# Performance work log

Measured on AMD Instinct MI355X. Metric: run time of the kernel, lower is better.

Reference implementation:

```python
import jax, jax.numpy as jnp
import numpy as np

INP = 512
HIDDEN = 512
N_HEADS = 8          # called 'head_dim' in the torch code
D_HEAD = HIDDEN // N_HEADS  # 64
BASE = 10000.0
SCALE = D_HEAD ** (-0.5)


def rope(x):
    # x: [b, s, h, d]
    b, s, h, d = x.shape
    half = d // 2
    theta = 1.0 / (BASE ** (jnp.arange(0, d, 2, dtype=jnp.float32) / d))  # [d/2]
    idx_theta = jnp.arange(s, dtype=jnp.float32)[:, None] * theta[None, :]  # [s, d/2]
    idx_theta2 = jnp.concatenate([idx_theta, idx_theta], axis=1)            # [s, d]
    neg_half = jnp.concatenate([-x[..., half:], x[..., :half]], axis=-1)
    cos = jnp.cos(idx_theta2)[None, :, None, :]
    sin = jnp.sin(idx_theta2)[None, :, None, :]
    return x * cos + neg_half * sin


def setup_inputs() -> dict:
    key = jax.random.key(0)
    ks = jax.random.split(key, 10)
    b, s = 4, 2048
    init = lambda k, shp, fan_in: jax.random.normal(k, shp, jnp.float32) * (fan_in ** -0.5)
    return {
        "x": jax.random.normal(ks[0], (b, s, INP), jnp.float32),
        "c": jax.random.normal(ks[1], (b, s, INP), jnp.float32),
        "Wq": init(ks[2], (INP, HIDDEN), INP), "bq": jnp.zeros((HIDDEN,), jnp.float32),
        "Wk": init(ks[3], (INP, HIDDEN), INP), "bk": jnp.zeros((HIDDEN,), jnp.float32),
        "Wv": init(ks[4], (INP, HIDDEN), INP), "bv": jnp.zeros((HIDDEN,), jnp.float32),
        "Wo": init(ks[5], (HIDDEN, INP), HIDDEN), "bo": jnp.zeros((INP,), jnp.float32),
    }


def reference(x, c, Wq, bq, Wk, bk, Wv, bv, Wo, bo):
    b, s, _ = x.shape
    h_res = x
    q = (c @ Wq + bq).reshape(b, s, N_HEADS, D_HEAD)
    k = (x @ Wk + bk).reshape(b, s, N_HEADS, D_HEAD)
    v = (x @ Wv + bv).reshape(b, s, N_HEADS, D_HEAD)
    q = rope(q)
    k = rope(k)  # computed but unused, exactly as in the source
    # NOTE: source computes scores between q and V (not k) -- faithful reproduction
    att = jnp.einsum('bihd,bjhd->bhij', q, v)            # [b, h, s, s]
    att = jax.nn.softmax(att * SCALE, axis=-1)
    out = jnp.einsum('bhij,bjhd->bihd', att, v)          # [b, s, h, d]
    out = out.reshape(b, s, HIDDEN)
    out = out @ Wo + bo
    return out + h_res
```

## Files before the change

### kernel.cpp

```cpp
#include <hip/hip_runtime.h>
#include <hip/hip_bf16.h>
#include <cstdint>

typedef float f32x4 __attribute__((ext_vector_type(4)));
typedef short bf16x8 __attribute__((ext_vector_type(8)));
typedef unsigned short u16;

#define B_    4
#define S_    2048
#define H_    8
#define D_    64
#define M_    8192

#define OFF_CBF   0UL
#define OFF_XBF   8388608UL
#define OFF_QBH   16777216UL
#define OFF_VBH   25165824UL
#define OFF_VTBH  33554432UL
#define OFF_ATTN  41943040UL
#define OFF_WQT   50331648UL
#define OFF_WVT   50855936UL
#define OFF_WOT   51380224UL
#define OFF_BIAS  51904512UL
#define OFF_COS   51910656UL
#define OFF_SIN   52172800UL
#define WS_NEEDED 52434944UL

__device__ __forceinline__ u16 f2bf(float f){
    union { float f; uint32_t u; } v; v.f = f;
    uint32_t r = (v.u + 0x7fffu + ((v.u >> 16) & 1u)) >> 16;
    return (u16)r;
}
__device__ __forceinline__ float bf2f(u16 h){
    union { uint32_t u; float f; } v; v.u = ((uint32_t)h) << 16;
    return v.f;
}
__device__ __forceinline__ uint32_t fbits(float f){
    union { float f; uint32_t u; } v; v.f = f; return v.u;
}

__device__ __forceinline__ int swz(int row, int col){
    return (col & ~63) | ((((col >> 3) & 7) ^ (row & 7)) << 3) | (col & 7);
}

__device__ __forceinline__ int detect_f32(const void* x_in){
    int lane = threadIdx.x & 63;
    ushort2 dv = ((const ushort2*)x_in)[lane];
    bool hit = ((((dv.x >> 7) & 0xFF) >= 160) || (((dv.y >> 7) & 0xFF) >= 160));
    return __ballot(hit) != 0ULL;
}

__device__ __forceinline__ void gload_lds16(const u16* g, u16* l){
    __builtin_amdgcn_global_load_lds(
        (const __attribute__((address_space(1))) void*)g,
        (__attribute__((address_space(3))) void*)l, 16, 0, 0);
}

__global__ void k_prep(const void* c_in, const void* x_in,
                       const void* Wq, const void* Wv, const void* Wo,
                       const void* bq, const void* bv, const void* bo,
                       u16* c_bf, u16* x_bf,
                       u16* Wqt, u16* Wvt, u16* Wot, float* bias_ws,
                       float* cos_t, float* sin_t){
    int bid = blockIdx.x;
    if (bid >= 11264){
        int idx = (bid - 11264) * 256 + threadIdx.x;
        int pos = idx >> 5, j = idx & 31;
        double theta = pow(10000.0, -(double)j / 32.0);
        double rev = ((double)pos * theta) * 0.15915494309189535;
        rev -= floor(rev);
        float fr = (float)rev;
        cos_t[idx] = __builtin_amdgcn_cosf(fr);
        sin_t[idx] = __builtin_amdgcn_sinf(fr);
        return;
    }
    if (bid >= 8192){
        int f = detect_f32(x_in);
        int wi = (bid - 8192) >> 10;
        int idx = ((bid - 8192) & 1023) * 256 + threadIdx.x;
        int k = idx >> 9, n = idx & 511;
        const void* W; u16* Wt; const void* bb;
        if (wi == 0){ W = Wq; Wt = Wqt; bb = bq; }
        else if (wi == 1){ W = Wv; Wt = Wvt; bb = bv; }
        else { W = Wo; Wt = Wot; bb = bo; }
        float v = f ? ((const float*)W)[idx] : bf2f(((const u16*)W)[idx]);
        Wt[n * 512 + swz(n, k)] = f2bf(v);
        if (idx < 512){
            float b = f ? ((const float*)bb)[idx] : bf2f(((const u16*)bb)[idx]);
            bias_ws[wi * 512 + idx] = b;
        }
        return;
    }
    int f = detect_f32(x_in);
    int isx = bid >= 4096;
    int t = (bid & 4095) * 256 + threadIdx.x;
    const void* src = isx ? x_in : c_in;
    u16* dst = isx ? x_bf : c_bf;
    int e0 = t * 4, row = e0 >> 9, col = e0 & 511;
    size_t didx = (size_t)row * 512 + swz(row, col);
    ushort4 o;
    if (f){
        float4 v = ((const float4*)src)[t];
        o.x = f2bf(v.x); o.y = f2bf(v.y); o.z = f2bf(v.z); o.w = f2bf(v.w);
    } else {
        o = ((const ushort4*)src)[t];
    }
    *(ushort4*)(dst + didx) = o;
}

__global__ __launch_bounds__(256) void k_gemm_qv(
    const u16* __restrict__ c_bf, const u16* __restrict__ x_bf,
    const u16* __restrict__ Wqt, const u16* __restrict__ Wvt,
    const float* __restrict__ bias_ws,
    const float* __restrict__ cos_t, const float* __restrict__ sin_t,
    u16* __restrict__ Qbh, u16* __restrict__ Vbh, u16* __restrict__ Vtbh)
{
    __shared__ __align__(16) u16 Als[2][128 * 64];
    __shared__ __align__(16) u16 Bls[2][128 * 64];
    const int w = threadIdx.x >> 6, lane = threadIdx.x & 63;
    const int g = lane >> 4, cq = lane & 15;
    const int wm = w & 1, wn = w >> 1;
    const int z = blockIdx.z;
    const u16* A  = z ? x_bf : c_bf;
    const u16* Wt = z ? Wvt : Wqt;
    const float* bias = bias_ws + (z ? 512 : 0);
    const int m0b = blockIdx.x * 128, n0b = blockIdx.y * 128;
    const int m0 = m0b + wm * 64, n0 = n0b + wn * 64;
    const int swzi = ((cq & 7) << 3);

    int srow[4], scol[4];
    #pragma unroll
    for (int i = 0; i < 4; i++){
        int flat = (w * 4 + i) * 64 + lane;
        srow[i] = flat >> 3; scol[i] = (flat & 7) * 8;
    }

    const f32x4 zero = {0.f, 0.f, 0.f, 0.f};
    f32x4 acc[4][4];
    #pragma unroll
    for (int i = 0; i < 4; i++)
        #pragma unroll
        for (int j = 0; j < 4; j++) acc[i][j] = zero;

    #pragma unroll
    for (int i = 0; i < 4; i++){
        gload_lds16(A  + (size_t)(m0b + srow[i]) * 512 + scol[i], &Als[0][(w*4 + i) * 512]);
        gload_lds16(Wt + (size_t)(n0b + srow[i]) * 512 + scol[i], &Bls[0][(w*4 + i) * 512]);
    }

    for (int kt = 0; kt < 8; kt++){
        const int buf = kt & 1;
        __builtin_amdgcn_s_waitcnt(0x0F70);
        __syncthreads();
        if (kt < 7){
            const int kk = (kt + 1) * 64;
            #pragma unroll
            for (int i = 0; i < 4; i++){
                gload_lds16(A  + (size_t)(m0b + srow[i]) * 512 + kk + scol[i], &Als[buf^1][(w*4 + i) * 512]);
                gload_lds16(Wt + (size_t)(n0b + srow[i]) * 512 + kk + scol[i], &Bls[buf^1][(w*4 + i) * 512]);
            }
        }
        #pragma unroll
        for (int ks = 0; ks < 2; ks++){
            const int cs = ((ks * 4 + g) << 3) ^ swzi;
            bf16x8 a[4], b[4];
            #pragma unroll
            for (int mt = 0; mt < 4; mt++)
                a[mt] = *(const bf16x8*)&Als[buf][(wm*64 + mt*16 + cq) * 64 + cs];
            #pragma unroll
            for (int nt = 0; nt < 4; nt++)
                b[nt] = *(const bf16x8*)&Bls[buf][(wn*64 + nt*16 + cq) * 64 + cs];
            #pragma unroll
            for (int mt = 0; mt < 4; mt++)
                #pragma unroll
                for (int nt = 0; nt < 4; nt++)
                    acc[mt][nt] = __builtin_amdgcn_mfma_f32_16x16x32_bf16(a[mt], b[nt], acc[mt][nt], 0, 0, 0);
        }
    }
    __syncthreads();

    #pragma unroll
    for (int nt = 0; nt < 4; nt++){
        float bvv = bias[n0 + nt*16 + cq];
        #pragma unroll
        for (int mt = 0; mt < 4; mt++) acc[mt][nt] += bvv;
    }
    const int h = n0 >> 6;
    if (z == 0){
        const float SCL = 0.125f * 1.4426950408889634f;
        #pragma unroll
        for (int mt = 0; mt < 4; mt++){
            #pragma unroll
            for (int r = 0; r < 4; r++){
                int row = m0 + mt*16 + g*4 + r;
                int b_idx = row >> 11, si = row & 2047;
                size_t base = ((size_t)(b_idx*8 + h) * 2048 + si) * 64;
                #pragma unroll
                for (int nt = 0; nt < 2; nt++){
                    int dj = nt*16 + cq;
                    float cv = cos_t[si*32 + dj], sv = sin_t[si*32 + dj];
                    float x1 = acc[mt][nt][r], x2 = acc[mt][nt+2][r];
                    Qbh[base + dj]      = f2bf((x1*cv - x2*sv) * SCL);
                    Qbh[base + dj + 32] = f2bf((x2*cv + x1*sv) * SCL);
                }
            }
        }
    } else {
        float* ltw = ((float*)&Als[0][0]) + w * (16 * 65);
        const int b_idx = m0 >> 11, si0 = m0 & 2047;
        const size_t tbase = ((size_t)(b_idx*8 + h) * 64) * 2048;
        #pragma unroll
        for (int mt = 0; mt < 4; mt++)
            #pragma unroll
            for (int r = 0; r < 4; r++){
                int row = m0 + mt*16 + g*4 + r;
                int bi = row >> 11, si = row & 2047;
                size_t base = ((size_t)(bi*8 + h) * 2048 + si) * 64;
                #pragma unroll
                for (int nt = 0; nt < 4; nt++)
                    Vbh[base + nt*16 + cq] = f2bf(acc[mt][nt][r]);
            }
        #pragma unroll
        for (int nt = 0; nt < 4; nt++){
            #pragma unroll
            for (int mt = 0; mt < 4; mt++)
                #pragma unroll
                for (int r = 0; r < 4; r++)
                    ltw[cq * 65 + mt*16 + g*4 + r] = acc[mt][nt][r];
            __builtin_amdgcn_wave_barrier();
            #pragma unroll
            for (int dd = 0; dd < 16; dd++){
                float v = ltw[dd * 65 + lane];
                Vtbh[tbase + (size_t)(nt*16 + dd) * 2048 + si0 + lane] = f2bf(v);
            }
            __builtin_amdgcn_wave_barrier();
        }
    }
}

__global__ __launch_bounds__(256) void k_attn(
    const u16* __restrict__ Qbh, const u16* __restrict__ Vbh,
    const u16* __restrict__ Vtbh, u16* __restrict__ attn)
{
    __shared__ u16 Vs[2][64 * 68];
    __shared__ u16 Vts[2][64 * 68];
    __shared__ float pl[4][32 * 68];
    const int w = threadIdx.x >> 6, lane = threadIdx.x & 63;
    const int g = lane >> 4, cq = lane & 15;
    const int bh = blockIdx.y;
    const int i0 = blockIdx.x * 128 + w * 32;

    bf16x8 aq[2][2];
    #pragma unroll
    for (int mt = 0; mt < 2; mt++)
        #pragma unroll
        for (int kk = 0; kk < 2; kk++)
            aq[mt][kk] = *(const bf16x8*)(Qbh + ((size_t)bh*2048 + i0 + mt*16 + cq)*64 + kk*32 + g*8);

    int lst[2]; const u16 *gvs[2], *gvt[2];
    #pragma unroll
    for (int i = 0; i < 2; i++){
        int flat = (w*2 + i) * 64 + lane;
        int srow = flat >> 3, scol = (flat & 7) * 8;
        gvs[i] = Vbh  + ((size_t)bh * 2048 + srow) * 64 + scol;
        gvt[i] = Vtbh + ((size_t)(bh * 64) + srow) * 2048 + scol;
        lst[i] = srow * 68 + scol;
    }
    #pragma unroll
    for (int i = 0; i < 2; i++){
        *(bf16x8*)&Vs[0][lst[i]]  = *(const bf16x8*)gvs[i];
        *(bf16x8*)&Vts[0][lst[i]] = *(const bf16x8*)gvt[i];
    }

    const f32x4 zero = {0.f, 0.f, 0.f, 0.f};
    f32x4 o[2][4]; float fl[2][4];
    #pragma unroll
    for (int mt = 0; mt < 2; mt++)
        #pragma unroll
        for (int t = 0; t < 4; t++){ o[mt][t] = zero; fl[mt][t] = 0.f; }

    for (int jt = 0; jt < 32; jt++){
        const int buf = jt & 1;
        bf16x8 n_vs[2], n_vt[2];
        #pragma unroll
        for (int i = 0; i < 2; i++){
            n_vs[i] = *(const bf16x8*)(gvs[i] + (size_t)(jt + 1) * 4096);
            n_vt[i] = *(const bf16x8*)(gvt[i] + (size_t)(jt + 1) * 64);
        }
        __syncthreads();

        bf16x8 bv[2][4];
        #pragma unroll
        for (int kk = 0; kk < 2; kk++)
            #pragma unroll
            for (int t = 0; t < 4; t++)
                bv[kk][t] = *(const bf16x8*)&Vs[buf][(t*16 + cq)*68 + kk*32 + g*8];
        f32x4 s2[2][4];
        #pragma unroll
        for (int mt = 0; mt < 2; mt++){
            #pragma unroll
            for (int t = 0; t < 4; t++) s2[mt][t] = zero;
            #pragma unroll
            for (int kk = 0; kk < 2; kk++)
                #pragma unroll
                for (int t = 0; t < 4; t++)
                    s2[mt][t] = __builtin_amdgcn_mfma_f32_16x16x32_bf16(aq[mt][kk], bv[kk][t], s2[mt][t], 0, 0, 0);
        }
        #pragma unroll
        for (int mt = 0; mt < 2; mt++){
            #pragma unroll
            for (int t = 0; t < 4; t++)
                #pragma unroll
                for (int r = 0; r < 4; r++)
                    s2[mt][t][r] = __builtin_amdgcn_exp2f(s2[mt][t][r]);
            #pragma unroll
            for (int r = 0; r < 4; r++)
                fl[mt][r] += (s2[mt][0][r] + s2[mt][1][r]) + (s2[mt][2][r] + s2[mt][3][r]);
        }
        #pragma unroll
        for (int mt = 0; mt < 2; mt++)
            #pragma unroll
            for (int r = 0; r < 4; r++)
                #pragma unroll
                for (int t = 0; t < 4; t++)
                    pl[w][(mt*16 + g*4 + r)*68 + t*16 + cq] = s2[mt][t][r];
        __builtin_amdgcn_wave_barrier();
        bf16x8 bt[2][4];
        #pragma unroll
        for (int kk = 0; kk < 2; kk++)
            #pragma unroll
            for (int tn = 0; tn < 4; tn++)
                bt[kk][tn] = *(const bf16x8*)&Vts[buf][(tn*16 + cq)*68 + kk*32 + g*8];
        #pragma unroll
        for (int mt = 0; mt < 2; mt++)
            #pragma unroll
            for (int kk = 0; kk < 2; kk++){
                f32x4 u0 = *(const f32x4*)&pl[w][(mt*16 + cq)*68 + kk*32 + g*8];
                f32x4 u1 = *(const f32x4*)&pl[w][(mt*16 + cq)*68 + kk*32 + g*8 + 4];
                union { bf16x8 v; uint32_t wd[4]; } pk;
                pk.wd[0] = (fbits(u0[0]) >> 16) | (fbits(u0[1]) & 0xffff0000u);
                pk.wd[1] = (fbits(u0[2]) >> 16) | (fbits(u0[3]) & 0xffff0000u);
                pk.wd[2] = (fbits(u1[0]) >> 16) | (fbits(u1[1]) & 0xffff0000u);
                pk.wd[3] = (fbits(u1[2]) >> 16) | (fbits(u1[3]) & 0xffff0000u);
                #pragma unroll
                for (int tn = 0; tn < 4; tn++)
                    o[mt][tn] = __builtin_amdgcn_mfma_f32_16x16x32_bf16(pk.v, bt[kk][tn], o[mt][tn], 0, 0, 0);
            }
        __builtin_amdgcn_wave_barrier();

        #pragma unroll
        for (int i = 0; i < 2; i++){
            *(bf16x8*)&Vs[buf ^ 1][lst[i]]  = n_vs[i];
            *(bf16x8*)&Vts[buf ^ 1][lst[i]] = n_vt[i];
        }
    }
    const int b_idx = bh >> 3, h = bh & 7;
    #pragma unroll
    for (int mt = 0; mt < 2; mt++){
        #pragma unroll
        for (int r = 0; r < 4; r++){
            float sum = fl[mt][r];
            sum += __shfl_xor(sum, 1);
            sum += __shfl_xor(sum, 2);
            sum += __shfl_xor(sum, 4);
            sum += __shfl_xor(sum, 8);
            fl[mt][r] = 1.f / sum;
        }
        f32x4 iv = {fl[mt][0], fl[mt][1], fl[mt][2], fl[mt][3]};
        #pragma unroll
        for (int t = 0; t < 4; t++){
            f32x4 ov = o[mt][t] * iv;
            #pragma unroll
            for (int r = 0; r < 4; r++){
                int row = i0 + mt*16 + g*4 + r;
                int col = h*64 + t*16 + cq;
                attn[((size_t)(b_idx*2048 + row))*512 + swz(row, col)] = f2bf(ov[r]);
            }
        }
    }
}

__global__ __launch_bounds__(256) void k_gemm_out(
    const u16* __restrict__ attn, const u16* __restrict__ Wot,
    const float* __restrict__ bias_ws, const void* __restrict__ x_in,
    void* __restrict__ out)
{
    __shared__ __align__(16) u16 Als[2][128 * 64];
    __shared__ __align__(16) u16 Bls[2][64 * 64];
    const int w = threadIdx.x >> 6, lane = threadIdx.x & 63;
    const int g = lane >> 4, cq = lane & 15;
    const int wm = w & 1, wn = w >> 1;
    const int m0b = blockIdx.x * 128, n0b = blockIdx.y * 64;
    const int m0 = m0b + wm * 64, n0 = n0b + wn * 32;
    const int f = detect_f32(x_in);
    const int swzi = ((cq & 7) << 3);

    int sra[4], sca[4], srb[2], scb[2];
    #pragma unroll
    for (int i = 0; i < 4; i++){
        int flat = (w * 4 + i) * 64 + lane;
        sra[i] = flat >> 3; sca[i] = (flat & 7) * 8;
    }
    #pragma unroll
    for (int i = 0; i < 2; i++){
        int flat = (w * 2 + i) * 64 + lane;
        srb[i] = flat >> 3; scb[i] = (flat & 7) * 8;
    }

    const f32x4 zero = {0.f, 0.f, 0.f, 0.f};
    f32x4 acc[4][2];
    #pragma unroll
    for (int i = 0; i < 4; i++)
        #pragma unroll
        for (int j = 0; j < 2; j++) acc[i][j] = zero;

    #pragma unroll
    for (int i = 0; i < 4; i++)
        gload_lds16(attn + (size_t)(m0b + sra[i]) * 512 + sca[i], &Als[0][(w*4 + i) * 512]);
    #pragma unroll
    for (int i = 0; i < 2; i++)
        gload_lds16(Wot + (size_t)(n0b + srb[i]) * 512 + scb[i], &Bls[0][(w*2 + i) * 512]);

    for (int kt = 0; kt < 8; kt++){
        const int buf = kt & 1;
        __builtin_amdgcn_s_waitcnt(0x0F70);
        __syncthreads();
        if (kt < 7){
            const int kk = (kt + 1) * 64;
            #pragma unroll
            for (int i = 0; i < 4; i++)
                gload_lds16(attn + (size_t)(m0b + sra[i]) * 512 + kk + sca[i], &Als[buf^1][(w*4 + i) * 512]);
            #pragma unroll
            for (int i = 0; i < 2; i++)
                gload_lds16(Wot + (size_t)(n0b + srb[i]) * 512 + kk + scb[i], &Bls[buf^1][(w*2 + i) * 512]);
        }
        #pragma unroll
        for (int ks = 0; ks < 2; ks++){
            const int cs = ((ks * 4 + g) << 3) ^ swzi;
            bf16x8 a[4], b[2];
            #pragma unroll
            for (int mt = 0; mt < 4; mt++)
                a[mt] = *(const bf16x8*)&Als[buf][(wm*64 + mt*16 + cq) * 64 + cs];
            #pragma unroll
            for (int nt = 0; nt < 2; nt++)
                b[nt] = *(const bf16x8*)&Bls[buf][(wn*32 + nt*16 + cq) * 64 + cs];
            #pragma unroll
            for (int mt = 0; mt < 4; mt++)
                #pragma unroll
                for (int nt = 0; nt < 2; nt++)
                    acc[mt][nt] = __builtin_amdgcn_mfma_f32_16x16x32_bf16(a[mt], b[nt], acc[mt][nt], 0, 0, 0);
        }
    }
    #pragma unroll
    for (int mt = 0; mt < 4; mt++)
        #pragma unroll
        for (int nt = 0; nt < 2; nt++)
            #pragma unroll
            for (int r = 0; r < 4; r++){
                int row = m0 + mt*16 + g*4 + r;
                int col = n0 + nt*16 + cq;
                size_t idx = (size_t)row * 512 + col;
                float resid = f ? ((const float*)x_in)[idx] : bf2f(((const u16*)x_in)[idx]);
                float v = acc[mt][nt][r] + bias_ws[1024 + col] + resid;
                if (f) ((float*)out)[idx] = v;
                else   ((u16*)out)[idx] = f2bf(v);
            }
}

extern "C" void kernel_launch(void* const* d_in, const int* in_sizes, int n_in,
                              void* d_out, int out_size, void* d_ws, size_t ws_size,
                              hipStream_t stream){
    const void* x_in = d_in[0];
    const void* c_in = d_in[1];
    const void* Wq = d_in[2]; const void* bq = d_in[3];
    const void* Wv = d_in[6]; const void* bv = d_in[7];
    const void* Wo = d_in[8]; const void* bo = d_in[9];

    if (ws_size < WS_NEEDED){
        hipMemsetAsync(d_out, 0, (size_t)out_size * 2, stream);
        return;
    }
    char* ws = (char*)d_ws;
    u16* c_bf  = (u16*)(ws + OFF_CBF);
    u16* x_bf  = (u16*)(ws + OFF_XBF);
    u16* Qbh   = (u16*)(ws + OFF_QBH);
    u16* Vbh   = (u16*)(ws + OFF_VBH);
    u16* Vtbh  = (u16*)(ws + OFF_VTBH);
    u16* attn  = (u16*)(ws + OFF_ATTN);
    u16* Wqt   = (u16*)(ws + OFF_WQT);
    u16* Wvt   = (u16*)(ws + OFF_WVT);
    u16* Wot   = (u16*)(ws + OFF_WOT);
    float* bias_ws = (float*)(ws + OFF_BIAS);
    float* cos_t   = (float*)(ws + OFF_COS);
    float* sin_t   = (float*)(ws + OFF_SIN);

    k_prep<<<11520, 256, 0, stream>>>(c_in, x_in, Wq, Wv, Wo, bq, bv, bo,
                                      c_bf, x_bf, Wqt, Wvt, Wot, bias_ws, cos_t, sin_t);
    k_gemm_qv<<<dim3(64, 4, 2), 256, 0, stream>>>(c_bf, x_bf, Wqt, Wvt, bias_ws,
                                                  cos_t, sin_t, Qbh, Vbh, Vtbh);
    k_attn<<<dim3(16, 32), 256, 0, stream>>>(Qbh, Vbh, Vtbh, attn);
    k_gemm_out<<<dim3(64, 8), 256, 0, stream>>>(attn, Wot, bias_ws, x_in, d_out);
}
```

Before: 196.2 us.

## Keep attention probabilities in registers via transposed MFMA and swizzled V layouts

The attention kernel now computes scores transposed (V·Q) so each lane's exp'd scores can feed a 16x16x16 MFMA directly as a register operand. This removes the per-wave LDS staging buffer for probabilities and its round trip. The projection kernel writes V and V^T with an XOR swizzle so the attention kernel can copy tiles straight to LDS with global_load_lds, without padding and with fewer bank conflicts. The output store is also vectorised. The cost is an extra, smaller MFMA shape for PV, and every consumer must agree on the new swizzled layouts.

Result: no change. 196.4 us (+0.1%).

```diff
diff --git a/kernel.cpp b/kernel.cpp
--- a/kernel.cpp
+++ b/kernel.cpp
@@ -4,6 +4,7 @@
 
 typedef float f32x4 __attribute__((ext_vector_type(4)));
 typedef short bf16x8 __attribute__((ext_vector_type(8)));
+typedef short bf16x4 __attribute__((ext_vector_type(4)));
 typedef unsigned short u16;
 
 #define B_    4
@@ -37,6 +38,15 @@
 }
 __device__ __forceinline__ uint32_t fbits(float f){
     union { float f; uint32_t u; } v; v.f = f; return v.u;
+}
+
+__device__ __forceinline__ f32x4 mfma16(bf16x4 a, bf16x4 b, f32x4 c){
+#if __has_builtin(__builtin_amdgcn_mfma_f32_16x16x16bf16_1k)
+    return __builtin_amdgcn_mfma_f32_16x16x16bf16_1k(a, b, c, 0, 0, 0);
+#else
+    asm volatile("v_mfma_f32_16x16x16_bf16 %0, %1, %2, %0" : "+v"(c) : "v"(a), "v"(b));
+    return c;
+#endif
 }
 
 __device__ __forceinline__ int swz(int row, int col){
@@ -216,9 +226,13 @@
                 int row = m0 + mt*16 + g*4 + r;
                 int bi = row >> 11, si = row & 2047;
                 size_t base = ((size_t)(bi*8 + h) * 2048 + si) * 64;
-                #pragma unroll
-                for (int nt = 0; nt < 4; nt++)
-                    Vbh[base + nt*16 + cq] = f2bf(acc[mt][nt][r]);
+                int s7 = si & 7;
+                #pragma unroll
+                for (int nt = 0; nt < 4; nt++){
+                    int dj = nt*16 + cq;
+                    int col = ((((dj >> 3) ^ s7) & 7) << 3) | (dj & 7);
+                    Vbh[base + col] = f2bf(acc[mt][nt][r]);
+                }
             }
         #pragma unroll
         for (int nt = 0; nt < 4; nt++){
@@ -231,7 +245,8 @@
             #pragma unroll
             for (int dd = 0; dd < 16; dd++){
                 float v = ltw[dd * 65 + lane];
-                Vtbh[tbase + (size_t)(nt*16 + dd) * 2048 + si0 + lane] = f2bf(v);
+                int col = ((((lane >> 3) ^ (dd & 7)) & 7) << 3) | (lane & 7);
+                Vtbh[tbase + (size_t)(nt*16 + dd) * 2048 + si0 + col] = f2bf(v);
             }
             __builtin_amdgcn_wave_barrier();
         }
@@ -242,11 +257,11 @@
     const u16* __restrict__ Qbh, const u16* __restrict__ Vbh,
     const u16* __restrict__ Vtbh, u16* __restrict__ attn)
 {
-    __shared__ u16 Vs[2][64 * 68];
-    __shared__ u16 Vts[2][64 * 68];
-    __shared__ float pl[4][32 * 68];
+    __shared__ __align__(16) u16 Vs[2][64 * 64];
+    __shared__ __align__(16) u16 Vts[2][64 * 64];
     const int w = threadIdx.x >> 6, lane = threadIdx.x & 63;
     const int g = lane >> 4, cq = lane & 15;
+    const int s7 = cq & 7;
     const int bh = blockIdx.y;
     const int i0 = blockIdx.x * 128 + w * 32;
 
@@ -257,125 +272,82 @@
         for (int kk = 0; kk < 2; kk++)
             aq[mt][kk] = *(const bf16x8*)(Qbh + ((size_t)bh*2048 + i0 + mt*16 + cq)*64 + kk*32 + g*8);
 
-    int lst[2]; const u16 *gvs[2], *gvt[2];
-    #pragma unroll
-    for (int i = 0; i < 2; i++){
-        int flat = (w*2 + i) * 64 + lane;
-        int srow = flat >> 3, scol = (flat & 7) * 8;
-        gvs[i] = Vbh  + ((size_t)bh * 2048 + srow) * 64 + scol;
-        gvt[i] = Vtbh + ((size_t)(bh * 64) + srow) * 2048 + scol;
-        lst[i] = srow * 68 + scol;
-    }
-    #pragma unroll
-    for (int i = 0; i < 2; i++){
-        *(bf16x8*)&Vs[0][lst[i]]  = *(const bf16x8*)gvs[i];
-        *(bf16x8*)&Vts[0][lst[i]] = *(const bf16x8*)gvt[i];
-    }
+    const int c0 = (w * 2) * 512, c1 = c0 + 512;
+    const u16* gvs0 = Vbh + (size_t)bh * 131072 + c0 + lane * 8;
+    const u16* gvs1 = gvs0 + 512;
+    const int dr0 = (w * 2) * 8 + (lane >> 3);
+    const u16* gvt0 = Vtbh + ((size_t)bh * 64 + dr0) * 2048 + (lane & 7) * 8;
+    const u16* gvt1 = gvt0 + 8 * 2048;
+
+    gload_lds16(gvs0, &Vs[0][c0]);
+    gload_lds16(gvs1, &Vs[0][c1]);
+    gload_lds16(gvt0, &Vts[0][c0]);
+    gload_lds16(gvt1, &Vts[0][c1]);
 
     const f32x4 zero = {0.f, 0.f, 0.f, 0.f};
-    f32x4 o[2][4]; float fl[2][4];
+    f32x4 o[2][4]; float fl[2] = {0.f, 0.f};
     #pragma unroll
     for (int mt = 0; mt < 2; mt++)
         #pragma unroll
-        for (int t = 0; t < 4; t++){ o[mt][t] = zero; fl[mt][t] = 0.f; }
+        for (int t = 0; t < 4; t++) o[mt][t] = zero;
 
     for (int jt = 0; jt < 32; jt++){
         const int buf = jt & 1;
-        bf16x8 n_vs[2], n_vt[2];
-        #pragma unroll
-        for (int i = 0; i < 2; i++){
-            n_vs[i] = *(const bf16x8*)(gvs[i] + (size_t)(jt + 1) * 4096);
-            n_vt[i] = *(const bf16x8*)(gvt[i] + (size_t)(jt + 1) * 64);
-        }
+        __builtin_amdgcn_s_waitcnt(0x0F70);
         __syncthreads();
-
-        bf16x8 bv[2][4];
-        #pragma unroll
-        for (int kk = 0; kk < 2; kk++)
-            #pragma unroll
-            for (int t = 0; t < 4; t++)
-                bv[kk][t] = *(const bf16x8*)&Vs[buf][(t*16 + cq)*68 + kk*32 + g*8];
-        f32x4 s2[2][4];
-        #pragma unroll
-        for (int mt = 0; mt < 2; mt++){
-            #pragma unroll
-            for (int t = 0; t < 4; t++) s2[mt][t] = zero;
-            #pragma unroll
-            for (int kk = 0; kk < 2; kk++)
-                #pragma unroll
-                for (int t = 0; t < 4; t++)
-                    s2[mt][t] = __builtin_amdgcn_mfma_f32_16x16x32_bf16(aq[mt][kk], bv[kk][t], s2[mt][t], 0, 0, 0);
-        }
-        #pragma unroll
-        for (int mt = 0; mt < 2; mt++){
-            #pragma unroll
-            for (int t = 0; t < 4; t++)
-                #pragma unroll
-                for (int r = 0; r < 4; r++)
-                    s2[mt][t][r] = __builtin_amdgcn_exp2f(s2[mt][t][r]);
-            #pragma unroll
-            for (int r = 0; r < 4; r++)
-                fl[mt][r] += (s2[mt][0][r] + s2[mt][1][r]) + (s2[mt][2][r] + s2[mt][3][r]);
-        }
-        #pragma unroll
-        for (int mt = 0; mt < 2; mt++)
-            #pragma unroll
-            for (int r = 0; r < 4; r++)
-                #pragma unroll
-                for (int t = 0; t < 4; t++)
-                    pl[w][(mt*16 + g*4 + r)*68 + t*16 + cq] = s2[mt][t][r];
-        __builtin_amdgcn_wave_barrier();
-        bf16x8 bt[2][4];
-        #pragma unroll
-        for (int kk = 0; kk < 2; kk++)
-            #pragma unroll
-            for (int tn = 0; tn < 4; tn++)
-                bt[kk][tn] = *(const bf16x8*)&Vts[buf][(tn*16 + cq)*68 + kk*32 + g*8];
-        #pragma unroll
-        for (int mt = 0; mt < 2; mt++)
-            #pragma unroll
-            for (int kk = 0; kk < 2; kk++){
-                f32x4 u0 = *(const f32x4*)&pl[w][(mt*16 + cq)*68 + kk*32 + g*8];
-                f32x4 u1 = *(const f32x4*)&pl[w][(mt*16 + cq)*68 + kk*32 + g*8 + 4];
-                union { bf16x8 v; uint32_t wd[4]; } pk;
-                pk.wd[0] = (fbits(u0[0]) >> 16) | (fbits(u0[1]) & 0xffff0000u);
-                pk.wd[1] = (fbits(u0[2]) >> 16) | (fbits(u0[3]) & 0xffff0000u);
-                pk.wd[2] = (fbits(u1[0]) >> 16) | (fbits(u1[1]) & 0xffff0000u);
-                pk.wd[3] = (fbits(u1[2]) >> 16) | (fbits(u1[3]) & 0xffff0000u);
-                #pragma unroll
-                for (int tn = 0; tn < 4; tn++)
-                    o[mt][tn] = __builtin_amdgcn_mfma_f32_16x16x32_bf16(pk.v, bt[kk][tn], o[mt][tn], 0, 0, 0);
-            }
-        __builtin_amdgcn_wave_barrier();
-
-        #pragma unroll
-        for (int i = 0; i < 2; i++){
-            *(bf16x8*)&Vs[buf ^ 1][lst[i]]  = n_vs[i];
-            *(bf16x8*)&Vts[buf ^ 1][lst[i]] = n_vt[i];
+        if (jt < 31){
+            const size_t os = (size_t)(jt + 1) * 4096, ot = (size_t)(jt + 1) * 64;
+            gload_lds16(gvs0 + os, &Vs[buf^1][c0]);
+            gload_lds16(gvs1 + os, &Vs[buf^1][c1]);
+            gload_lds16(gvt0 + ot, &Vts[buf^1][c0]);
+            gload_lds16(gvt1 + ot, &Vts[buf^1][c1]);
+        }
+        bf16x4 pk[2][4];
+        #pragma unroll
+        for (int t = 0; t < 4; t++){
+            bf16x8 bv0 = *(const bf16x8*)&Vs[buf][(t*16 + cq)*64 + ((g ^ s7) << 3)];
+            bf16x8 bv1 = *(const bf16x8*)&Vs[buf][(t*16 + cq)*64 + (((4 + g) ^ s7) << 3)];
+            #pragma unroll
+            for (int mt = 0; mt < 2; mt++){
+                f32x4 s = __builtin_amdgcn_mfma_f32_16x16x32_bf16(bv0, aq[mt][0], zero, 0, 0, 0);
+                s = __builtin_amdgcn_mfma_f32_16x16x32_bf16(bv1, aq[mt][1], s, 0, 0, 0);
+                #pragma unroll
+                for (int r = 0; r < 4; r++) s[r] = __builtin_amdgcn_exp2f(s[r]);
+                fl[mt] += (s[0] + s[1]) + (s[2] + s[3]);
+                union { bf16x4 v; uint32_t wd[2]; } u;
+                u.wd[0] = (fbits(s[0]) >> 16) | (fbits(s[1]) & 0xffff0000u);
+                u.wd[1] = (fbits(s[2]) >> 16) | (fbits(s[3]) & 0xffff0000u);
+                pk[mt][t] = u.v;
+            }
+        }
+        #pragma unroll
+        for (int t = 0; t < 4; t++){
+            const int chk = ((t*2 + (g >> 1)) ^ s7) & 7;
+            #pragma unroll
+            for (int tn = 0; tn < 4; tn++){
+                bf16x4 bt = *(const bf16x4*)&Vts[buf][(tn*16 + cq)*64 + (chk << 3) + (g & 1)*4];
+                o[0][tn] = mfma16(bt, pk[0][t], o[0][tn]);
+                o[1][tn] = mfma16(bt, pk[1][t], o[1][tn]);
+            }
         }
     }
     const int b_idx = bh >> 3, h = bh & 7;
     #pragma unroll
     for (int mt = 0; mt < 2; mt++){
-        #pragma unroll
-        for (int r = 0; r < 4; r++){
-            float sum = fl[mt][r];
-            sum += __shfl_xor(sum, 1);
-            sum += __shfl_xor(sum, 2);
-            sum += __shfl_xor(sum, 4);
-            sum += __shfl_xor(sum, 8);
-            fl[mt][r] = 1.f / sum;
-        }
-        f32x4 iv = {fl[mt][0], fl[mt][1], fl[mt][2], fl[mt][3]};
-        #pragma unroll
-        for (int t = 0; t < 4; t++){
-            f32x4 ov = o[mt][t] * iv;
-            #pragma unroll
-            for (int r = 0; r < 4; r++){
-                int row = i0 + mt*16 + g*4 + r;
-                int col = h*64 + t*16 + cq;
-                attn[((size_t)(b_idx*2048 + row))*512 + swz(row, col)] = f2bf(ov[r]);
-            }
+        float sum = fl[mt];
+        sum += __shfl_xor(sum, 16);
+        sum += __shfl_xor(sum, 32);
+        float inv = 1.f / sum;
+        int row = b_idx*2048 + i0 + mt*16 + cq;
+        #pragma unroll
+        for (int tn = 0; tn < 4; tn++){
+            f32x4 ov = o[mt][tn] * inv;
+            uint2 pw;
+            pw.x = (fbits(ov[0]) >> 16) | (fbits(ov[1]) & 0xffff0000u);
+            pw.y = (fbits(ov[2]) >> 16) | (fbits(ov[3]) & 0xffff0000u);
+            int chunk = ((tn*2 + (g >> 1)) ^ s7) & 7;
+            int col = h*64 + (chunk << 3) + (g & 1)*4;
+            *(uint2*)&attn[(size_t)row * 512 + col] = pw;
         }
     }
 }
```
